# Optimization experiments

Measured on AMD Instinct MI355X. Metric: run time of the kernel, lower is better.

Reference implementation:

```python
import jax, jax.numpy as jnp
import numpy as np

D_MODEL = 1024
D_INNER = 2048   # expand * d_model
D_STATE = 16
D_CONV = 4
DT_RANK = 64     # ceil(d_model / 16)
BATCH = 4
SEQ = 4096


def setup_inputs() -> dict:
    key = jax.random.key(0)
    ks = jax.random.split(key, 8)
    nrm = lambda k, shape, scale: jax.random.normal(k, shape, jnp.float32) * scale
    # dt_proj bias init (inverse softplus of dt in [dt_min, dt_max])
    dt_min, dt_max, dt_floor = 1e-3, 1e-1, 1e-4
    dt = jnp.exp(jax.random.uniform(ks[5], (D_INNER,), jnp.float32)
                 * (np.log(dt_max) - np.log(dt_min)) + np.log(dt_min))
    dt = jnp.clip(dt, dt_floor, None)
    b_dt = dt + jnp.log(-jnp.expm1(-dt))
    # A = diag(1..d_state) per channel, stored as log
    A_log = jnp.broadcast_to(jnp.log(jnp.arange(1, D_STATE + 1, dtype=jnp.float32))[None, :],
                             (D_INNER, D_STATE)).copy()
    dt_std = DT_RANK ** -0.5
    return {
        "x": nrm(ks[0], (BATCH, SEQ, D_MODEL), 1.0),
        "W_in": nrm(ks[1], (2 * D_INNER, D_MODEL), 0.02),
        "conv_w": nrm(ks[2], (D_INNER, 1, D_CONV), 0.2),
        "conv_b": jnp.zeros((D_INNER,), jnp.float32),
        "W_x": nrm(ks[3], (DT_RANK + 2 * D_STATE, D_INNER), 0.02),
        "W_dt": jax.random.uniform(ks[4], (D_INNER, DT_RANK), jnp.float32, -dt_std, dt_std),
        "b_dt": b_dt,
        "A_log": A_log,
        "D": jnp.ones((D_INNER,), jnp.float32),
        "W_out": nrm(ks[6], (D_MODEL, D_INNER), 0.02),
    }


def reference(x, W_in, conv_w, conv_b, W_x, W_dt, b_dt, A_log, D, W_out):
    B, T, _ = x.shape
    silu = jax.nn.silu
    # in_proj -> (x_inner, z)
    xz = jnp.einsum('btd,ed->bte', x, W_in)          # (B,T,2*d_inner)
    x_inner, z = jnp.split(xz, 2, axis=-1)
    # causal depthwise conv1d (pad left d_conv-1, equiv to torch pad+slice[:T])
    xp = jnp.pad(x_inner.transpose(0, 2, 1), ((0, 0), (0, 0), (D_CONV - 1, 0)))
    xc = jax.lax.conv_general_dilated(xp, conv_w, (1,), 'VALID',
                                      feature_group_count=D_INNER)  # (B,d_inner,T)
    x_conv = silu(xc + conv_b[None, :, None]).transpose(0, 2, 1)    # (B,T,d_inner)
    # x_proj -> dt_rank | B | C
    x_dbl = jnp.einsum('btd,ed->bte', x_conv, W_x)
    dt_r, B_ssm, C_ssm = jnp.split(x_dbl, [DT_RANK, DT_RANK + D_STATE], axis=-1)
    dt = jax.nn.softplus(jnp.einsum('btr,dr->btd', dt_r, W_dt) + b_dt)  # (B,T,d_inner)
    A = -jnp.exp(A_log)                                                 # (d_inner,d_state)
    # selective scan over time
    def step(s, inp):
        x_t, dt_t, B_t, C_t = inp              # (B,d_inner),(B,d_inner),(B,d_state),(B,d_state)
        dA = jnp.exp(dt_t[:, :, None] * A[None])              # (B,d_inner,d_state)
        s = s * dA + (dt_t * x_t)[:, :, None] * B_t[:, None, :]
        y_t = jnp.einsum('bds,bs->bd', s, C_t)
        return s, y_t

    s0 = jnp.zeros((B, D_INNER, D_STATE), jnp.float32)
    scan_in = (x_conv.transpose(1, 0, 2), dt.transpose(1, 0, 2),
               B_ssm.transpose(1, 0, 2), C_ssm.transpose(1, 0, 2))
    _, ys = jax.lax.scan(step, s0, scan_in)    # (T,B,d_inner)
    y = ys.transpose(1, 0, 2)
    y = y * silu(z) + D * x_conv
    out = jnp.einsum('btd,ed->bte', y, W_out)  # (B,T,d_model)
    return out
```

## Files before the change

### kernel.cpp

```cpp
#include <hip/hip_runtime.h>
#include <hip/hip_bf16.h>
#include <hip/hip_fp16.h>

#define SEQ    4096
#define DMODEL 1024
#define DINNER 2048
#define DSTATE 16
#define DTRANK 64
#define NC     32
#define CL     128
#define SPLITK 4

typedef __bf16 v8bf  __attribute__((ext_vector_type(8)));
typedef float  f32x4 __attribute__((ext_vector_type(4)));
typedef unsigned short u16x8 __attribute__((ext_vector_type(8)));

static __device__ __forceinline__ float bfu2f(unsigned short u) {
    union { float f; unsigned int i; } c; c.i = ((unsigned int)u) << 16; return c.f;
}
static __device__ __forceinline__ unsigned short f2bfu(float f) {
    union { float f; unsigned int i; } c; c.f = f;
    unsigned int r = c.i + 0x7FFFu + ((c.i >> 16) & 1u);
    return (unsigned short)(r >> 16);
}
static __device__ __forceinline__ float softplus_fast(float v) {
    return fmaxf(v, 0.f) + __logf(1.f + __expf(-fabsf(v)));
}

static __device__ __forceinline__ void gload_lds16(const void* g, void* l) {
    __builtin_amdgcn_global_load_lds(
        (const __attribute__((address_space(1))) unsigned int*)g,
        (__attribute__((address_space(3))) unsigned int*)l, 16, 0, 0);
}

static __device__ __forceinline__ void pow16(float e1, float* pw) {
    const float e2 = e1 * e1, e4 = e2 * e2, e8 = e4 * e4;
    pw[0] = e1;        pw[1] = e2;        pw[2] = e2 * e1;   pw[3] = e4;
    pw[4] = e4 * e1;   pw[5] = e4 * e2;   pw[6] = e4 * pw[2]; pw[7] = e8;
    pw[8] = e8 * e1;   pw[9] = e8 * e2;   pw[10] = e8 * pw[2]; pw[11] = e8 * e4;
    pw[12] = e8 * pw[4]; pw[13] = e8 * pw[5]; pw[14] = e8 * pw[6]; pw[15] = e8 * e8;
}

__global__ void detect_kernel(const void* __restrict__ x, int* __restrict__ flag)
{
    const float f = ((const float*)x)[threadIdx.x];
    const float a = fabsf(f);
    const bool ok = (a < 1e20f) && (a > 1e-20f);
    unsigned long long m = __ballot(ok);
    if (threadIdx.x == 0) *flag = (__popcll(m) >= 48) ? 1 : 0;
}

__global__ void prep_kernel(const unsigned short* __restrict__ a_log_b,
                            int* __restrict__ sflag)
{
    __shared__ int ok_sh;
    if (threadIdx.x == 0) ok_sh = 1;
    __syncthreads();
    int ok = 1;
    for (int i = threadIdx.x; i < DINNER * DSTATE; i += 256) {
        const float A = __expf(bfu2f(a_log_b[i]));
        const float n = (float)((i & 15) + 1);
        if (fabsf(A - n) > 0.02f * n) ok = 0;
    }
    if (!ok) atomicAnd(&ok_sh, 0);
    __syncthreads();
    if (threadIdx.x == 0) *sflag = ok_sh;
}

__global__ __launch_bounds__(256) void cvt_kernel(
    const void* __restrict__ src, size_t src_off,
    unsigned short* __restrict__ dst, int n, const int* __restrict__ flagp)
{
    const int f32 = *flagp;
    const int stride = gridDim.x * 256;
    if (f32) {
        const float* s = (const float*)src + src_off;
        for (int i = blockIdx.x * 256 + threadIdx.x; i < n; i += stride)
            dst[i] = f2bfu(s[i]);
    } else {
        const unsigned short* s = (const unsigned short*)src + src_off;
        for (int i = blockIdx.x * 256 + threadIdx.x; i < n; i += stride)
            dst[i] = s[i];
    }
}

__global__ __launch_bounds__(256) void gemm_db(
    const unsigned short* __restrict__ A, int lda,
    const unsigned short* __restrict__ B, int ldb,
    void* __restrict__ Cbase, int row0c, int ldc, int c_ext,
    int N, int K, const int* __restrict__ flagp)
{
    __shared__ __align__(16) unsigned short SM[4 * 128 * 64];

    const int cf32 = c_ext ? *flagp : 0;

    const int tid  = threadIdx.x;
    const int lane = tid & 63;
    const int wave = tid >> 6;
    const int wr   = wave >> 1;
    const int wc   = wave & 1;

    const int nwg = gridDim.x * gridDim.y;
    const int bid = blockIdx.y * gridDim.x + blockIdx.x;
    const int swz = (bid & 7) * (nwg >> 3) + (bid >> 3);
    const int m0  = (swz / gridDim.x) * 128;
    const int n0  = (swz % gridDim.x) * 128;

    f32x4 acc[4][4] = {};

    const int r32 = tid >> 3;
    const int c8  = tid & 7;

    const unsigned short* Arow = A + (size_t)m0 * lda;
    const unsigned short* Brow = B + (size_t)n0 * ldb;

#define STAGE_DB(buf, k0)                                                      \
    {                                                                          \
        _Pragma("unroll")                                                      \
        for (int h = 0; h < 4; ++h) {                                          \
            const int rr = r32 + h * 32;                                       \
            const int lg = (c8 ^ (rr & 7)) * 8;                                \
            gload_lds16(&Arow[(size_t)rr * lda + (k0) + lg],                   \
                        &SM[(buf) * 8192 + rr * 64 + c8 * 8]);                 \
            gload_lds16(&Brow[(size_t)rr * ldb + (k0) + lg],                   \
                        &SM[16384 + (buf) * 8192 + rr * 64 + c8 * 8]);         \
        }                                                                      \
    }

    STAGE_DB(0, 0);
    const int NT = K >> 6;
    int cur = 0;

    for (int kt = 0; kt < NT; ++kt) {
        if (kt + 1 < NT) {
            STAGE_DB(cur ^ 1, (kt + 1) * 64);
            asm volatile("s_waitcnt vmcnt(8)" ::: "memory");
        } else {
            asm volatile("s_waitcnt vmcnt(0)" ::: "memory");
        }
        __builtin_amdgcn_s_barrier();

        const unsigned short* Ab = &SM[cur * 8192];
        const unsigned short* Bb = &SM[16384 + cur * 8192];
        const int lm = lane & 15;
        const int g  = lane >> 4;
#pragma unroll
        for (int ks = 0; ks < 2; ++ks) {
            v8bf a_frag[4], b_frag[4];
#pragma unroll
            for (int i = 0; i < 4; ++i) {
                const int ra = wr * 64 + i * 16 + lm;
                const int rb = wc * 64 + i * 16 + lm;
                a_frag[i] = *reinterpret_cast<const v8bf*>(
                    &Ab[ra * 64 + (((ks * 4 + g) ^ (ra & 7))) * 8]);
                b_frag[i] = *reinterpret_cast<const v8bf*>(
                    &Bb[rb * 64 + (((ks * 4 + g) ^ (rb & 7))) * 8]);
            }
#pragma unroll
            for (int i = 0; i < 4; ++i)
#pragma unroll
                for (int j = 0; j < 4; ++j)
                    acc[i][j] = __builtin_amdgcn_mfma_f32_16x16x32_bf16(
                        a_frag[i], b_frag[j], acc[i][j], 0, 0, 0);
        }
        asm volatile("" ::: "memory");
        __builtin_amdgcn_s_barrier();
        cur ^= 1;
    }
#undef STAGE_DB

    float* eb = reinterpret_cast<float*>(SM);
    {
        const int lm = lane & 15;
        const int lr = (lane >> 4) * 4;
#pragma unroll
        for (int i = 0; i < 4; ++i)
#pragma unroll
            for (int j = 0; j < 4; ++j) {
                const int cl = wc * 64 + j * 16 + lm;
#pragma unroll
                for (int q = 0; q < 4; ++q) {
                    const int row = wr * 64 + i * 16 + lr + q;
                    eb[row * 128 + (cl ^ ((row & 7) << 2))] = acc[i][j][q];
                }
            }
    }
    __syncthreads();
#pragma unroll
    for (int r0 = 0; r0 < 8; ++r0) {
        const int row = (tid >> 4) + r0 * 16;
        const int cb2 = (tid & 15) * 8;
        const int sw  = (row & 7) << 2;
        const f32x4 v0 = *reinterpret_cast<const f32x4*>(&eb[row * 128 + (cb2 ^ sw)]);
        const f32x4 v1 = *reinterpret_cast<const f32x4*>(&eb[row * 128 + ((cb2 + 4) ^ sw)]);
        const size_t gr = (size_t)(row0c + m0 + row) * ldc + n0 + cb2;
        if (cf32) {
            __builtin_nontemporal_store(v0, reinterpret_cast<f32x4*>(&((float*)Cbase)[gr]));
            __builtin_nontemporal_store(v1, reinterpret_cast<f32x4*>(&((float*)Cbase)[gr + 4]));
        } else {
            u16x8 o;
#pragma unroll
            for (int k = 0; k < 4; ++k) { o[k] = f2bfu(v0[k]); o[4 + k] = f2bfu(v1[k]); }
            *reinterpret_cast<u16x8*>(&((unsigned short*)Cbase)[gr]) = o;
        }
    }
}

__global__ __launch_bounds__(256) void gemm_dt(
    const unsigned short* __restrict__ A, int lda,
    const unsigned short* __restrict__ B, int ldb,
    __half* __restrict__ Cbase, int ldc,
    const unsigned short* __restrict__ bias)
{
    __shared__ __align__(16) unsigned short As[128 * 64];
    __shared__ __align__(16) unsigned short Bs[128 * 64];

    const int tid  = threadIdx.x;
    const int lane = tid & 63;
    const int wave = tid >> 6;
    const int wr   = wave >> 1;
    const int wc   = wave & 1;
    const int m0   = blockIdx.y * 128;
    const int n0   = blockIdx.x * 128;

    f32x4 acc[4][4] = {};

    const int r32 = tid >> 3;
    const int c8  = tid & 7;

    {
#pragma unroll
        for (int h = 0; h < 4; ++h) {
            const int rr = r32 + h * 32;
            const int lg = (c8 ^ (rr & 7)) * 8;
            gload_lds16(&A[(size_t)(m0 + rr) * lda + lg], &As[rr * 64 + c8 * 8]);
            gload_lds16(&B[(size_t)(n0 + rr) * ldb + lg], &Bs[rr * 64 + c8 * 8]);
        }
        __syncthreads();

        const int lm = lane & 15;
        const int g  = lane >> 4;
#pragma unroll
        for (int ks = 0; ks < 2; ++ks) {
            v8bf a_frag[4], b_frag[4];
#pragma unroll
            for (int i = 0; i < 4; ++i) {
                const int ra = wr * 64 + i * 16 + lm;
                const int rb = wc * 64 + i * 16 + lm;
                a_frag[i] = *reinterpret_cast<const v8bf*>(
                    &As[ra * 64 + (((ks * 4 + g) ^ (ra & 7))) * 8]);
                b_frag[i] = *reinterpret_cast<const v8bf*>(
                    &Bs[rb * 64 + (((ks * 4 + g) ^ (rb & 7))) * 8]);
            }
#pragma unroll
            for (int i = 0; i < 4; ++i)
#pragma unroll
                for (int j = 0; j < 4; ++j)
                    acc[i][j] = __builtin_amdgcn_mfma_f32_16x16x32_bf16(
                        a_frag[i], b_frag[j], acc[i][j], 0, 0, 0);
        }
    }

    const int lm = lane & 15;
    const int lr = (lane >> 4) * 4;
#pragma unroll
    for (int i = 0; i < 4; ++i) {
#pragma unroll
        for (int j = 0; j < 4; ++j) {
            const int col = n0 + wc * 64 + j * 16 + lm;
            const float bv = bfu2f(bias[col]);
#pragma unroll
            for (int q = 0; q < 4; ++q) {
                const int row = m0 + wr * 64 + i * 16 + lr + q;
                Cbase[(size_t)row * ldc + col] =
                    __float2half(softplus_fast(acc[i][j][q] + bv));
            }
        }
    }
}

__global__ __launch_bounds__(256) void gemm_splitk(
    const unsigned short* __restrict__ A, int lda,
    const unsigned short* __restrict__ B, int ldb,
    float* __restrict__ part, int Mrows,
    int N, int kchunk)
{
    __shared__ __align__(16) unsigned short As[128 * 64];
    __shared__ __align__(16) unsigned short Bs[128 * 64];

    const int tid  = threadIdx.x;
    const int lane = tid & 63;
    const int wave = tid >> 6;
    const int wr   = wave >> 1;
    const int wc   = wave & 1;
    const int m0   = blockIdx.y * 128;
    const int split = blockIdx.z;
    const int kbeg = split * kchunk;

    f32x4 acc[4][4] = {};

    const int r32 = tid >> 3;
    const int c8  = tid & 7;

    for (int k0 = kbeg; k0 < kbeg + kchunk; k0 += 64) {
        __syncthreads();
#pragma unroll
        for (int h = 0; h < 4; ++h) {
            const int rr = r32 + h * 32;
            const int lg = (c8 ^ (rr & 7)) * 8;
            gload_lds16(&A[(size_t)(m0 + rr) * lda + k0 + lg], &As[rr * 64 + c8 * 8]);
            gload_lds16(&B[(size_t)rr * ldb + k0 + lg], &Bs[rr * 64 + c8 * 8]);
        }
        __syncthreads();

        const int lm = lane & 15;
        const int g  = lane >> 4;
#pragma unroll
        for (int ks = 0; ks < 2; ++ks) {
            v8bf a_frag[4], b_frag[4];
#pragma unroll
            for (int i = 0; i < 4; ++i) {
                const int ra = wr * 64 + i * 16 + lm;
                const int rb = wc * 64 + i * 16 + lm;
                a_frag[i] = *reinterpret_cast<const v8bf*>(
                    &As[ra * 64 + (((ks * 4 + g) ^ (ra & 7))) * 8]);
                b_frag[i] = *reinterpret_cast<const v8bf*>(
                    &Bs[rb * 64 + (((ks * 4 + g) ^ (rb & 7))) * 8]);
            }
#pragma unroll
            for (int i = 0; i < 4; ++i)
#pragma unroll
                for (int j = 0; j < 4; ++j)
                    acc[i][j] = __builtin_amdgcn_mfma_f32_16x16x32_bf16(
                        a_frag[i], b_frag[j], acc[i][j], 0, 0, 0);
        }
    }

    const int lm = lane & 15;
    const int lr = (lane >> 4) * 4;
    float* dst = part + (size_t)split * Mrows * 96;
#pragma unroll
    for (int i = 0; i < 4; ++i) {
#pragma unroll
        for (int j = 0; j < 4; ++j) {
            const int col = wc * 64 + j * 16 + lm;
            if (col >= N) continue;
#pragma unroll
            for (int q = 0; q < 4; ++q) {
                const int row = m0 + wr * 64 + i * 16 + lr + q;
                dst[(size_t)row * 96 + col] = acc[i][j][q];
            }
        }
    }
}

__global__ __launch_bounds__(256) void splitk_reduce(
    const float* __restrict__ part, unsigned short* __restrict__ dst,
    float* __restrict__ bcf, int n)
{
    const int i = blockIdx.x * 256 + threadIdx.x;
    if (i >= n) return;
    float s = 0.f;
#pragma unroll
    for (int k = 0; k < SPLITK; ++k) s += part[(size_t)k * n + i];
    dst[i] = f2bfu(s);
    const int m = i / 96;
    const int col = i - m * 96;
    if (col >= 64) bcf[(size_t)m * 32 + (col - 64)] = s;
}

__global__ __launch_bounds__(256) void conv_silu_kernel(
    const unsigned short* __restrict__ xz,
    const unsigned short* __restrict__ cw,
    const unsigned short* __restrict__ cb,
    unsigned short* __restrict__ xc)
{
    const int idx = blockIdx.x * 256 + threadIdx.x;
    const int d2 = idx & 1023;
    const int m = idx >> 10;
    const int t = m & (SEQ - 1);
    const int d = d2 * 2;

    const u16x8 w = *reinterpret_cast<const u16x8*>(&cw[d * 4]);
    const unsigned int bb = *reinterpret_cast<const unsigned int*>(&cb[d]);
    float s0 = bfu2f((unsigned short)(bb & 0xffff));
    float s1 = bfu2f((unsigned short)(bb >> 16));
#pragma unroll
    for (int j = 0; j < 4; ++j) {
        const int tt = t - 3 + j;
        if (tt >= 0) {
            const unsigned int xv = *reinterpret_cast<const unsigned int*>(
                &xz[(size_t)(m - 3 + j) * 4096 + d]);
            s0 += bfu2f(w[j])     * bfu2f((unsigned short)(xv & 0xffff));
            s1 += bfu2f(w[4 + j]) * bfu2f((unsigned short)(xv >> 16));
        }
    }
    const float g0 = s0 / (1.f + __expf(-s0));
    const float g1 = s1 / (1.f + __expf(-s1));
    const unsigned int o = (unsigned int)f2bfu(g0) | ((unsigned int)f2bfu(g1) << 16);
    *reinterpret_cast<unsigned int*>(&xc[(size_t)m * 2048 + d]) = o;
}

__global__ __launch_bounds__(256) void scan_local_kernel(
    const unsigned short* __restrict__ xz,
    const unsigned short* __restrict__ xconv,
    const float* __restrict__ bcf,
    const unsigned short* __restrict__ A_log,
    float* __restrict__ S,
    float* __restrict__ sumdt,
    const int* __restrict__ sflagp)
{
    const int gid = blockIdx.x * 256 + threadIdx.x;
    const int d = gid & (DINNER - 1);
    const int c = (gid >> 11) & (NC - 1);
    const int b = gid >> 16;
    const int fast = *sflagp;

    float st[16];
#pragma unroll
    for (int s = 0; s < 16; ++s) st[s] = 0.f;
    float sd = 0.f;
    const size_t mb = (size_t)b * SEQ + c * CL;

    float Ar[16];
    if (!fast) {
#pragma unroll
        for (int s = 0; s < 16; ++s) Ar[s] = -__expf(bfu2f(A_log[d * DSTATE + s]));
    }

    for (int t = 0; t < CL; ++t) {
        const size_t m = mb + t;
        const float dt = __half2float(
            reinterpret_cast<const __half*>(xz)[m * 4096 + d]);
        const float x  = bfu2f(xconv[m * DINNER + d]);
        const f32x4 B0 = *reinterpret_cast<const f32x4*>(&bcf[m * 32]);
        const f32x4 B1 = *reinterpret_cast<const f32x4*>(&bcf[m * 32 + 4]);
        const f32x4 B2 = *reinterpret_cast<const f32x4*>(&bcf[m * 32 + 8]);
        const f32x4 B3 = *reinterpret_cast<const f32x4*>(&bcf[m * 32 + 12]);
        const float du = dt * x;
        float pw[16];
        if (fast) {
            pow16(__expf(-dt), pw);
        } else {
#pragma unroll
            for (int s = 0; s < 16; ++s) pw[s] = __expf(dt * Ar[s]);
        }
#pragma unroll
        for (int s = 0; s < 4; ++s) st[s]      = st[s]      * pw[s]      + du * B0[s];
#pragma unroll
        for (int s = 0; s < 4; ++s) st[4 + s]  = st[4 + s]  * pw[4 + s]  + du * B1[s];
#pragma unroll
        for (int s = 0; s < 4; ++s) st[8 + s]  = st[8 + s]  * pw[8 + s]  + du * B2[s];
#pragma unroll
        for (int s = 0; s < 4; ++s) st[12 + s] = st[12 + s] * pw[12 + s] + du * B3[s];
        sd += dt;
    }
    const size_t o = (((size_t)b * NC + c) * DINNER + d) * DSTATE;
#pragma unroll
    for (int s = 0; s < 16; s += 4) {
        f32x4 v = { st[s], st[s + 1], st[s + 2], st[s + 3] };
        *reinterpret_cast<f32x4*>(&S[o + s]) = v;
    }
    sumdt[((size_t)b * NC + c) * DINNER + d] = sd;
}

__global__ __launch_bounds__(256) void scan_carry_kernel(
    const unsigned short* __restrict__ A_log,
    float* __restrict__ S,
    const float* __restrict__ sumdt)
{
    const int gid = blockIdx.x * 256 + threadIdx.x;
    const int s = gid & 15;
    const int d = (gid >> 4) & (DINNER - 1);
    const int b = gid >> 15;

    const float A = -__expf(bfu2f(A_log[d * DSTATE + s]));
    float carry = 0.f;
    for (int c = 0; c < NC; ++c) {
        const size_t o = (((size_t)b * NC + c) * DINNER + d) * DSTATE + s;
        const float se = S[o];
        S[o] = carry;
        carry = carry * __expf(A * sumdt[((size_t)b * NC + c) * DINNER + d]) + se;
    }
}

__global__ __launch_bounds__(256) void scan_final_kernel(
    unsigned short* __restrict__ xz,
    const unsigned short* __restrict__ xconv,
    const float* __restrict__ bcf,
    const unsigned short* __restrict__ A_log,
    const unsigned short* __restrict__ Dvec,
    const float* __restrict__ S,
    const int* __restrict__ sflagp)
{
    const int gid = blockIdx.x * 256 + threadIdx.x;
    const int d = gid & (DINNER - 1);
    const int c = (gid >> 11) & (NC - 1);
    const int b = gid >> 16;
    const int fast = *sflagp;

    const float Dv = bfu2f(Dvec[d]);
    float st[16];
    const size_t o = (((size_t)b * NC + c) * DINNER + d) * DSTATE;
#pragma unroll
    for (int s = 0; s < 16; s += 4) {
        f32x4 v = *reinterpret_cast<const f32x4*>(&S[o + s]);
        st[s] = v[0]; st[s + 1] = v[1]; st[s + 2] = v[2]; st[s + 3] = v[3];
    }
    const size_t mb = (size_t)b * SEQ + c * CL;

    float Ar[16];
    if (!fast) {
#pragma unroll
        for (int s = 0; s < 16; ++s) Ar[s] = -__expf(bfu2f(A_log[d * DSTATE + s]));
    }

    for (int t = 0; t < CL; ++t) {
        const size_t m = mb + t;
        const float dt = __half2float(
            reinterpret_cast<const __half*>(xz)[m * 4096 + d]);
        const float x  = bfu2f(xconv[m * DINNER + d]);
        const f32x4 B0 = *reinterpret_cast<const f32x4*>(&bcf[m * 32]);
        const f32x4 B1 = *reinterpret_cast<const f32x4*>(&bcf[m * 32 + 4]);
        const f32x4 B2 = *reinterpret_cast<const f32x4*>(&bcf[m * 32 + 8]);
        const f32x4 B3 = *reinterpret_cast<const f32x4*>(&bcf[m * 32 + 12]);
        const f32x4 C0 = *reinterpret_cast<const f32x4*>(&bcf[m * 32 + 16]);
        const f32x4 C1 = *reinterpret_cast<const f32x4*>(&bcf[m * 32 + 20]);
        const f32x4 C2 = *reinterpret_cast<const f32x4*>(&bcf[m * 32 + 24]);
        const f32x4 C3 = *reinterpret_cast<const f32x4*>(&bcf[m * 32 + 28]);
        const float du = dt * x;
        float pw[16];
        if (fast) {
            pow16(__expf(-dt), pw);
        } else {
#pragma unroll
            for (int s = 0; s < 16; ++s) pw[s] = __expf(dt * Ar[s]);
        }
        float p0 = 0.f, p1 = 0.f, p2 = 0.f, p3 = 0.f;
#pragma unroll
        for (int s = 0; s < 4; ++s) {
            st[s] = st[s] * pw[s] + du * B0[s];           p0 += st[s] * C0[s];
        }
#pragma unroll
        for (int s = 0; s < 4; ++s) {
            st[4 + s] = st[4 + s] * pw[4 + s] + du * B1[s];   p1 += st[4 + s] * C1[s];
        }
#pragma unroll
        for (int s = 0; s < 4; ++s) {
            st[8 + s] = st[8 + s] * pw[8 + s] + du * B2[s];   p2 += st[8 + s] * C2[s];
        }
#pragma unroll
        for (int s = 0; s < 4; ++s) {
            st[12 + s] = st[12 + s] * pw[12 + s] + du * B3[s]; p3 += st[12 + s] * C3[s];
        }
        const float p = (p0 + p1) + (p2 + p3);
        const float z = bfu2f(xz[m * 4096 + DINNER + d]);
        const float sig = 1.f / (1.f + __expf(-z));
        xz[m * 4096 + d] = f2bfu(p * (z * sig) + Dv * x);
    }
}

extern "C" void kernel_launch(void* const* d_in, const int* in_sizes, int n_in,
                              void* d_out, int out_size, void* d_ws, size_t ws_size,
                              hipStream_t stream)
{
    const void* x     = d_in[0];
    const void* W_in  = d_in[1];
    const void* convw = d_in[2];
    const void* convb = d_in[3];
    const void* W_x   = d_in[4];
    const void* W_dt  = d_in[5];
    const void* b_dt  = d_in[6];
    const void* A_log = d_in[7];
    const void* Dv    = d_in[8];
    const void* W_out = d_in[9];

    char* ws = (char*)d_ws;
    size_t off = 256;
    int* flag  = (int*)ws;
    int* sflag = (int*)ws + 16;
    auto arena = [&](size_t bytes) {
        char* p = ws + off;
        off += (bytes + 255) & ~(size_t)255;
        return p;
    };
    unsigned short* w_in_b  = (unsigned short*)arena((size_t)4096 * 1024 * 2);
    unsigned short* convw_b = (unsigned short*)arena(8192 * 2);
    unsigned short* convb_b = (unsigned short*)arena(2048 * 2);
    unsigned short* w_x_b   = (unsigned short*)arena((size_t)96 * 2048 * 2);
    unsigned short* w_dt_b  = (unsigned short*)arena((size_t)2048 * 64 * 2);
    unsigned short* b_dt_b  = (unsigned short*)arena(2048 * 2);
    unsigned short* a_log_b = (unsigned short*)arena((size_t)2048 * 16 * 2);
    unsigned short* dv_b    = (unsigned short*)arena(2048 * 2);
    unsigned short* w_out_b = (unsigned short*)arena((size_t)1024 * 2048 * 2);
    const size_t fixed = off;

    const size_t U_per_b  = (size_t)SEQ * 1024 * 2;
    const size_t per_batch =
        (size_t)SEQ * 4096 * 2 + (size_t)SEQ * 2048 * 2 + (size_t)SEQ * 96 * 2 +
        U_per_b;
    int CB = 4;
    while (CB > 1 && fixed + (size_t)CB * per_batch > ws_size) CB >>= 1;
    const int nchunks = 4 / CB;
    const int Mc = CB * SEQ;

    unsigned short* xz    = (unsigned short*)(ws + fixed);
    unsigned short* xconv = xz + (size_t)Mc * 4096;
    unsigned short* xdbl  = xconv + (size_t)Mc * 2048;
    char*           U     = (char*)(xdbl + (size_t)Mc * 96);
    unsigned short* x_bf  = (unsigned short*)U;
    float*          xpart = (float*)U;
    float*          bcf   = (float*)(U + (size_t)SPLITK * Mc * 96 * 4);
    float*          S     = (float*)U;
    float*          sumdt = (float*)(U + (size_t)CB * NC * 2048 * DSTATE * 4);

    detect_kernel<<<1, 64, 0, stream>>>(x, flag);

    cvt_kernel<<<1024, 256, 0, stream>>>(W_in,  0, w_in_b,  4096 * 1024, flag);
    cvt_kernel<<<32,   256, 0, stream>>>(convw, 0, convw_b, 8192,        flag);
    cvt_kernel<<<8,    256, 0, stream>>>(convb, 0, convb_b, 2048,        flag);
    cvt_kernel<<<256,  256, 0, stream>>>(W_x,   0, w_x_b,   96 * 2048,   flag);
    cvt_kernel<<<256,  256, 0, stream>>>(W_dt,  0, w_dt_b,  2048 * 64,   flag);
    cvt_kernel<<<8,    256, 0, stream>>>(b_dt,  0, b_dt_b,  2048,        flag);
    cvt_kernel<<<64,   256, 0, stream>>>(A_log, 0, a_log_b, 2048 * 16,   flag);
    cvt_kernel<<<8,    256, 0, stream>>>(Dv,    0, dv_b,    2048,        flag);
    cvt_kernel<<<1024, 256, 0, stream>>>(W_out, 0, w_out_b, 1024 * 2048, flag);
    prep_kernel<<<1, 256, 0, stream>>>(a_log_b, sflag);

    for (int cchunk = 0; cchunk < nchunks; ++cchunk) {
        const int row0 = cchunk * Mc;

        cvt_kernel<<<4096, 256, 0, stream>>>(
            x, (size_t)row0 * DMODEL, x_bf, Mc * DMODEL, flag);

        gemm_db<<<dim3(4096 / 128, Mc / 128), 256, 0, stream>>>(
            x_bf, DMODEL, w_in_b, DMODEL, xz, 0, 4096, 0, 4096, DMODEL, flag);

        conv_silu_kernel<<<(Mc * DINNER) / 512, 256, 0, stream>>>(
            xz, convw_b, convb_b, xconv);

        gemm_splitk<<<dim3(1, Mc / 128, SPLITK), 256, 0, stream>>>(
            xconv, DINNER, w_x_b, DINNER, xpart, Mc, 96, DINNER / SPLITK);
        splitk_reduce<<<(Mc * 96 + 255) / 256, 256, 0, stream>>>(
            xpart, xdbl, bcf, Mc * 96);

        gemm_dt<<<dim3(DINNER / 128, Mc / 128), 256, 0, stream>>>(
            xdbl, 96, w_dt_b, DTRANK, (__half*)xz, 4096, b_dt_b);

        scan_local_kernel<<<(CB * NC * DINNER) / 256, 256, 0, stream>>>(
            xz, xconv, bcf, a_log_b, S, sumdt, sflag);
        scan_carry_kernel<<<(CB * DINNER * DSTATE) / 256, 256, 0, stream>>>(
            a_log_b, S, sumdt);
        scan_final_kernel<<<(CB * NC * DINNER) / 256, 256, 0, stream>>>(
            xz, xconv, bcf, a_log_b, dv_b, S, sflag);

        gemm_db<<<dim3(DMODEL / 128, Mc / 128), 256, 0, stream>>>(
            xz, 4096, w_out_b, DINNER, d_out, row0, DMODEL, 1,
            DMODEL, DINNER, flag);
    }
}
```

Before: 710.9 us.

## Double scan chunk count and store inter-chunk states in fp16

The chunked selective scan now uses 64 chunks of 64 timesteps instead of 32 chunks of 128. This doubles the threads in the local and final scan kernels and halves each thread's serial loop length. The per-chunk state buffer is stored as fp16 rather than fp32, which keeps the workspace size unchanged and halves the traffic for writing, carrying and reloading it. The carry pass becomes twice as long, and fp16 storage of the states loses precision and could overflow or underflow for large state values.

Measured after the change: 696.6 us. 1.02x faster.

```diff
diff --git a/kernel.cpp b/kernel.cpp
--- a/kernel.cpp
+++ b/kernel.cpp
@@ -7,8 +7,8 @@
 #define DINNER 2048
 #define DSTATE 16
 #define DTRANK 64
-#define NC     32
-#define CL     128
+#define NC     64
+#define CL     64
 #define SPLITK 4
 
 typedef __bf16 v8bf  __attribute__((ext_vector_type(8)));
@@ -22,6 +22,12 @@
     union { float f; unsigned int i; } c; c.f = f;
     unsigned int r = c.i + 0x7FFFu + ((c.i >> 16) & 1u);
     return (unsigned short)(r >> 16);
+}
+static __device__ __forceinline__ float h2f(unsigned short u) {
+    __half h; *reinterpret_cast<unsigned short*>(&h) = u; return __half2float(h);
+}
+static __device__ __forceinline__ unsigned short f2h(float f) {
+    __half h = __float2half(f); return *reinterpret_cast<unsigned short*>(&h);
 }
 static __device__ __forceinline__ float softplus_fast(float v) {
     return fmaxf(v, 0.f) + __logf(1.f + __expf(-fabsf(v)));
@@ -406,14 +412,14 @@
     const unsigned short* __restrict__ xconv,
     const float* __restrict__ bcf,
     const unsigned short* __restrict__ A_log,
-    float* __restrict__ S,
+    unsigned short* __restrict__ S,
     float* __restrict__ sumdt,
     const int* __restrict__ sflagp)
 {
     const int gid = blockIdx.x * 256 + threadIdx.x;
     const int d = gid & (DINNER - 1);
     const int c = (gid >> 11) & (NC - 1);
-    const int b = gid >> 16;
+    const int b = gid >> 17;
     const int fast = *sflagp;
 
     float st[16];
@@ -456,17 +462,17 @@
         sd += dt;
     }
     const size_t o = (((size_t)b * NC + c) * DINNER + d) * DSTATE;
-#pragma unroll
-    for (int s = 0; s < 16; s += 4) {
-        f32x4 v = { st[s], st[s + 1], st[s + 2], st[s + 3] };
-        *reinterpret_cast<f32x4*>(&S[o + s]) = v;
-    }
+    u16x8 h0, h1;
+#pragma unroll
+    for (int s = 0; s < 8; ++s) { h0[s] = f2h(st[s]); h1[s] = f2h(st[8 + s]); }
+    *reinterpret_cast<u16x8*>(&S[o]) = h0;
+    *reinterpret_cast<u16x8*>(&S[o + 8]) = h1;
     sumdt[((size_t)b * NC + c) * DINNER + d] = sd;
 }
 
 __global__ __launch_bounds__(256) void scan_carry_kernel(
     const unsigned short* __restrict__ A_log,
-    float* __restrict__ S,
+    unsigned short* __restrict__ S,
     const float* __restrict__ sumdt)
 {
     const int gid = blockIdx.x * 256 + threadIdx.x;
@@ -478,8 +484,8 @@
     float carry = 0.f;
     for (int c = 0; c < NC; ++c) {
         const size_t o = (((size_t)b * NC + c) * DINNER + d) * DSTATE + s;
-        const float se = S[o];
-        S[o] = carry;
+        const float se = h2f(S[o]);
+        S[o] = f2h(carry);
         carry = carry * __expf(A * sumdt[((size_t)b * NC + c) * DINNER + d]) + se;
     }
 }
@@ -490,22 +496,23 @@
     const float* __restrict__ bcf,
     const unsigned short* __restrict__ A_log,
     const unsigned short* __restrict__ Dvec,
-    const float* __restrict__ S,
+    const unsigned short* __restrict__ S,
     const int* __restrict__ sflagp)
 {
     const int gid = blockIdx.x * 256 + threadIdx.x;
     const int d = gid & (DINNER - 1);
     const int c = (gid >> 11) & (NC - 1);
-    const int b = gid >> 16;
+    const int b = gid >> 17;
     const int fast = *sflagp;
 
     const float Dv = bfu2f(Dvec[d]);
     float st[16];
     const size_t o = (((size_t)b * NC + c) * DINNER + d) * DSTATE;
-#pragma unroll
-    for (int s = 0; s < 16; s += 4) {
-        f32x4 v = *reinterpret_cast<const f32x4*>(&S[o + s]);
-        st[s] = v[0]; st[s + 1] = v[1]; st[s + 2] = v[2]; st[s + 3] = v[3];
+    {
+        const u16x8 h0 = *reinterpret_cast<const u16x8*>(&S[o]);
+        const u16x8 h1 = *reinterpret_cast<const u16x8*>(&S[o + 8]);
+#pragma unroll
+        for (int s = 0; s < 8; ++s) { st[s] = h2f(h0[s]); st[8 + s] = h2f(h1[s]); }
     }
     const size_t mb = (size_t)b * SEQ + c * CL;
 
@@ -611,8 +618,8 @@
     unsigned short* x_bf  = (unsigned short*)U;
     float*          xpart = (float*)U;
     float*          bcf   = (float*)(U + (size_t)SPLITK * Mc * 96 * 4);
-    float*          S     = (float*)U;
-    float*          sumdt = (float*)(U + (size_t)CB * NC * 2048 * DSTATE * 4);
+    unsigned short* S     = (unsigned short*)U;
+    float*          sumdt = (float*)(U + (size_t)CB * NC * 2048 * DSTATE * 2);
 
     detect_kernel<<<1, 64, 0, stream>>>(x, flag);
 
```
